# Optimization experiments

Measured on AMD Instinct MI355X. Metric: run time of the kernel, lower is better.

The kernel has to match this reference:

```python
import jax, jax.numpy as jnp
import numpy as np
from jax import lax

N_OBJ = 21   # 20 VOC classes + background
N_ACT = 27   # HICO actions
HUMAN = 14   # index of 'human' in VOC_BBOX_LABEL_NAMES
ROI_SZ = 7
SCALE = 1.0 / 16.0
STD = (0.1, 0.1, 0.2, 0.2)
MEAN = (0.0, 0.0, 0.0, 0.0)
SIGMA = 0.3
NMS_T = 0.0  # thresh passed to non_maximum_suppression in source
EPS = 1e-3
NEG = -1e30


def setup_inputs():
    key = jax.random.key(0)
    ks = jax.random.split(key, 9)
    R = 2000
    C, Hf, Wf = 512, 38, 50
    Himg, Wimg = 608, 800
    x = jax.random.normal(ks[0], (1, C, Hf, Wf), dtype=jnp.float32)
    pred_scores = jax.random.normal(ks[1], (R, N_OBJ), dtype=jnp.float32)
    pred_off = 0.5 * jax.random.normal(ks[2], (R, N_OBJ * 4), dtype=jnp.float32)
    ys = jnp.sort(jax.random.uniform(ks[3], (R, 2), minval=0.0, maxval=Himg - 1.0), axis=1)
    xs = jnp.sort(jax.random.uniform(ks[4], (R, 2), minval=0.0, maxval=Wimg - 1.0), axis=1)
    rois = jnp.stack([ys[:, 0], xs[:, 0], ys[:, 1] + 1.0, xs[:, 1] + 1.0], axis=1)  # [R,4] yxyx, image coords
    D = C * ROI_SZ * ROI_SZ  # 25088
    W1 = jax.random.normal(ks[5], (D, 4096), dtype=jnp.float32) / np.float32(np.sqrt(D))
    b1 = jnp.zeros((4096,), jnp.float32)
    W2 = jax.random.normal(ks[6], (4096, 4096), dtype=jnp.float32) / 64.0
    b2 = jnp.zeros((4096,), jnp.float32)
    W_loc = jax.random.normal(ks[7], (4096, 4), dtype=jnp.float32) / 64.0
    b_loc = jnp.zeros((4,), jnp.float32)
    W_act = jax.random.normal(ks[8], (4096, N_ACT), dtype=jnp.float32) / 64.0
    b_act = jnp.zeros((N_ACT,), jnp.float32)
    imgshape = jnp.array([Himg, Wimg], dtype=jnp.int32)
    return {"x": x, "pred_scores": pred_scores, "pred_off": pred_off, "rois": rois,
            "imgshape": imgshape, "W1": W1, "b1": b1, "W2": W2, "b2": b2,
            "W_loc": W_loc, "b_loc": b_loc, "W_act": W_act, "b_act": b_act}


def loc2bbox(src, loc):
    # src, loc: [...,4] (y1,x1,y2,x2) / (dy,dx,dh,dw)
    h = src[..., 2] - src[..., 0]
    w = src[..., 3] - src[..., 1]
    cy = src[..., 0] + 0.5 * h
    cx = src[..., 1] + 0.5 * w
    cy2 = loc[..., 0] * h + cy
    cx2 = loc[..., 1] * w + cx
    h2 = jnp.exp(loc[..., 2]) * h
    w2 = jnp.exp(loc[..., 3]) * w
    return jnp.stack([cy2 - 0.5 * h2, cx2 - 0.5 * w2, cy2 + 0.5 * h2, cx2 + 0.5 * w2], axis=-1)


def nms_keep(boxes, scores):
    # chainercv-style greedy NMS: suppress if IoU with an already-kept box >= NMS_T
    R = boxes.shape[0]
    order = jnp.argsort(-scores)
    b = boxes[order]
    tl = jnp.maximum(b[:, None, :2], b[None, :, :2])
    br = jnp.minimum(b[:, None, 2:], b[None, :, 2:])
    inter = jnp.prod(jnp.maximum(br - tl, 0.0), axis=-1)
    area = jnp.prod(jnp.maximum(b[:, 2:] - b[:, :2], 0.0), axis=-1)
    iou = inter / (area[:, None] + area[None, :] - inter + 1e-12)
    idx = jnp.arange(R)
    def body(i, keep):
        sup = jnp.any((iou[i] >= NMS_T) & keep & (idx < i))
        return keep.at[i].set(~sup)
    keep_sorted = lax.fori_loop(0, R, body, jnp.ones((R,), bool))
    return jnp.zeros((R,), bool).at[order].set(keep_sorted)


def roi_pool(feat, box_yxyx):
    # chainer RoIPooling2D on one roi; roi fed as [x1,y1,x2,y2] then scaled by SCALE
    C, Hf, Wf = feat.shape
    y1, x1, y2, x2 = box_yxyx[0], box_yxyx[1], box_yxyx[2], box_yxyx[3]
    xmin = jnp.round(x1 * SCALE).astype(jnp.int32)
    ymin = jnp.round(y1 * SCALE).astype(jnp.int32)
    xmax = jnp.round(x2 * SCALE).astype(jnp.int32)
    ymax = jnp.round(y2 * SCALE).astype(jnp.int32)
    rw = jnp.maximum(xmax - xmin + 1, 1).astype(jnp.float32)
    rh = jnp.maximum(ymax - ymin + 1, 1).astype(jnp.float32)
    p = jnp.arange(ROI_SZ, dtype=jnp.float32)
    hstart = jnp.clip(ymin + jnp.floor(p * rh / ROI_SZ).astype(jnp.int32), 0, Hf)
    hend = jnp.clip(ymin + jnp.ceil((p + 1.0) * rh / ROI_SZ).astype(jnp.int32), 0, Hf)
    wstart = jnp.clip(xmin + jnp.floor(p * rw / ROI_SZ).astype(jnp.int32), 0, Wf)
    wend = jnp.clip(xmin + jnp.ceil((p + 1.0) * rw / ROI_SZ).astype(jnp.int32), 0, Wf)
    r = jnp.arange(Hf)
    c = jnp.arange(Wf)
    rowm = (r[None, :] >= hstart[:, None]) & (r[None, :] < hend[:, None])  # [7,Hf]
    colm = (c[None, :] >= wstart[:, None]) & (c[None, :] < wend[:, None])  # [7,Wf]
    t = jnp.where(colm[None, None, :, :], feat[:, :, None, :], NEG).max(axis=-1)  # [C,Hf,7]
    out = jnp.where(rowm[None, :, :, None], t[:, None, :, :], NEG).max(axis=2)    # [C,7,7]
    return jnp.where(out <= NEG * 0.5, 0.0, out)


def xywh(b):
    # quirky encoding used in forward: x=(b3-b1)/2, y=(b2-b0)/2, w=b3-b1, h=b2-b0
    w = b[..., 3] - b[..., 1]
    h = b[..., 2] - b[..., 0]
    return jnp.stack([0.5 * w, 0.5 * h, w, h], axis=-1)


def reference(x, pred_scores, pred_off, rois, imgshape, W1, b1, W2, b2, W_loc, b_loc, W_act, b_act):
    Hf, Wf = x.shape[2], x.shape[3]
    R = rois.shape[0]
    img = imgshape.astype(jnp.float32)
    my_scale = Hf / img[0]
    sy = Hf / img[0]
    sx = Wf / img[1]
    roi = rois * jnp.stack([sy, sx, sy, sx])  # resize_bbox(image -> feature)
    std = jnp.tile(jnp.asarray(STD, jnp.float32), (N_OBJ,))
    mean = jnp.tile(jnp.asarray(MEAN, jnp.float32), (N_OBJ,))
    loc = (pred_off * std + mean).reshape(R, N_OBJ, 4)
    src = jnp.broadcast_to(roi[:, None, :], loc.shape)
    cb = loc2bbox(src, loc)  # [R,21,4]
    yc = jnp.clip(cb[..., 0::2], 0.0, float(Hf))
    xc = jnp.clip(cb[..., 1::2], 0.0, float(Wf))
    cls_bbox = jnp.stack([yc[..., 0], xc[..., 0], yc[..., 1], xc[..., 1]], axis=-1)
    prob = jax.nn.softmax(pred_scores, axis=1)  # strictly > 0, so prob>0 mask keeps all
    boxes_c = jnp.swapaxes(cls_bbox[:, 1:, :], 0, 1)  # [20,R,4]
    scores_c = prob[:, 1:].T                          # [20,R]
    keep = jax.vmap(nms_keep)(boxes_c, scores_c)      # [20,R] bool
    bbox_all = boxes_c.reshape(-1, 4)
    score_all = scores_c.reshape(-1)
    label_all = jnp.repeat(jnp.arange(N_OBJ - 1), R)
    kept = keep.reshape(-1)
    # get_pred_human_box: best-scoring kept box with label 'human'
    hmask = kept & (label_all == HUMAN)
    hi = jnp.argmax(jnp.where(hmask, score_all, -1.0))
    human_box = bbox_all[hi]  # feature coords, yxyx
    # RoI pool + classifier heads
    pool = roi_pool(x[0], human_box)
    feat = pool.reshape(1, -1)  # [1, 25088]
    fc7 = jax.nn.relu(jax.nn.relu(feat @ W1 + b1) @ W2 + b2)
    pred_object_loc = fc7 @ W_loc + b_loc   # [1,4]
    action_scores = fc7 @ W_act + b_act     # [1,27]
    # test-mode: gaussian over relative box encodings to pick object
    h4 = xywh(human_box)
    mu = xywh(pred_object_loc[0])
    cand = xywh(bbox_all)  # [20R,4]
    hw = jnp.maximum(h4[2], EPS)
    hh = jnp.maximum(h4[3], EPS)
    cw = jnp.maximum(cand[:, 2], EPS)
    ch = jnp.maximum(cand[:, 3], EPS)
    boh = jnp.stack([(cand[:, 0] - h4[0]) / hw, (cand[:, 1] - h4[1]) / hh,
                     jnp.log(cw / hw), jnp.log(ch / hh)], axis=-1)
    gau = jnp.exp(-jnp.sum((boh - mu) ** 2, axis=-1) / (2.0 * SIGMA * SIGMA))
    vmask = kept & (label_all != HUMAN)
    bi = jnp.argmax(jnp.where(vmask, gau, -1.0))
    obj_box = bbox_all[bi]
    # resize back to image coords (flip_bbox treated as identity)
    inv = jnp.stack([img[0] / Hf, img[1] / Wf, img[0] / Hf, img[1] / Wf])
    pred_human_box = (human_box * inv)[None, :]
    pred_obj_box = (obj_box * inv)[None, :]
    return pred_human_box, pred_obj_box, action_scores, my_scale
```

## Files before the change

### kernel.cpp

```cpp
#include <hip/hip_runtime.h>
#include <math.h>

#define R_ROIS 2000
#define NOBJ   21
#define NACT   27
#define HUMAN  14
#define CFEAT  512
#define HF     38
#define WF     50
#define DFEAT  (CFEAT*7*7)
#define H1DIM  4096

#define WS_LOGZ   0
#define WS_KEPT   2000
#define WS_FEAT   2080
#define WS_H1     27168
#define WS_H1R    31264
#define WS_FC7    35360
#define WS_FC7R   39456
#define WS_LOC    43552
#define WS_ACT    43556

__global__ void k_init(float* h1, float* fc7) {
    int i = blockIdx.x * blockDim.x + threadIdx.x;
    if (i < H1DIM) { h1[i] = 0.f; fc7[i] = 0.f; }
}

__global__ void k_logz(const float* __restrict__ scores, float* __restrict__ logZ) {
    int r = blockIdx.x * blockDim.x + threadIdx.x;
    if (r >= R_ROIS) return;
    const float* s = scores + r * NOBJ;
    float m = s[0];
    #pragma unroll
    for (int c = 1; c < NOBJ; ++c) m = fmaxf(m, s[c]);
    float sum = 0.f;
    #pragma unroll
    for (int c = 0; c < NOBJ; ++c) sum += expf(s[c] - m);
    logZ[r] = m + logf(sum);
}

__global__ void k_class_top(const float* __restrict__ scores, const float* __restrict__ logZ,
                            const float* __restrict__ off, const float* __restrict__ rois,
                            const int* __restrict__ imgshape, float* __restrict__ kept_box) {
    int cls = blockIdx.x + 1;
    __shared__ float sval[256];
    __shared__ int   sidx[256];
    float best = -1e30f; int bidx = 0x7fffffff;
    for (int r = threadIdx.x; r < R_ROIS; r += 256) {
        float v = scores[r * NOBJ + cls] - logZ[r];
        if (v > best) { best = v; bidx = r; }
    }
    sval[threadIdx.x] = best; sidx[threadIdx.x] = bidx;
    __syncthreads();
    for (int s = 128; s > 0; s >>= 1) {
        if (threadIdx.x < s) {
            float ov = sval[threadIdx.x + s]; int oi = sidx[threadIdx.x + s];
            if (ov > sval[threadIdx.x] ||
                (ov == sval[threadIdx.x] && oi < sidx[threadIdx.x])) {
                sval[threadIdx.x] = ov; sidx[threadIdx.x] = oi;
            }
        }
        __syncthreads();
    }
    if (threadIdx.x == 0) {
        int r = sidx[0];
        float Himg = (float)imgshape[0], Wimg = (float)imgshape[1];
        float sy = (float)HF / Himg, sx = (float)WF / Wimg;
        float y1 = rois[r*4+0]*sy, x1 = rois[r*4+1]*sx;
        float y2 = rois[r*4+2]*sy, x2 = rois[r*4+3]*sx;
        float dy = off[r*(NOBJ*4) + cls*4+0] * 0.1f;
        float dx = off[r*(NOBJ*4) + cls*4+1] * 0.1f;
        float dh = off[r*(NOBJ*4) + cls*4+2] * 0.2f;
        float dw = off[r*(NOBJ*4) + cls*4+3] * 0.2f;
        float h = y2 - y1, w = x2 - x1;
        float cy = y1 + 0.5f*h, cx = x1 + 0.5f*w;
        float cy2 = dy*h + cy, cx2 = dx*w + cx;
        float h2 = expf(dh)*h, w2 = expf(dw)*w;
        float by1 = fminf(fmaxf(cy2 - 0.5f*h2, 0.f), (float)HF);
        float bx1 = fminf(fmaxf(cx2 - 0.5f*w2, 0.f), (float)WF);
        float by2 = fminf(fmaxf(cy2 + 0.5f*h2, 0.f), (float)HF);
        float bx2 = fminf(fmaxf(cx2 + 0.5f*w2, 0.f), (float)WF);
        int l = cls - 1;
        kept_box[l*4+0] = by1; kept_box[l*4+1] = bx1;
        kept_box[l*4+2] = by2; kept_box[l*4+3] = bx2;
    }
}

__global__ void k_roipool(const float* __restrict__ x, const float* __restrict__ kept_box,
                          float* __restrict__ feat) {
    int idx = blockIdx.x * blockDim.x + threadIdx.x;
    if (idx >= DFEAT) return;
    float y1 = kept_box[HUMAN*4+0], x1 = kept_box[HUMAN*4+1];
    float y2 = kept_box[HUMAN*4+2], x2 = kept_box[HUMAN*4+3];
    int xmin = (int)rintf(x1 * 0.0625f);
    int ymin = (int)rintf(y1 * 0.0625f);
    int xmax = (int)rintf(x2 * 0.0625f);
    int ymax = (int)rintf(y2 * 0.0625f);
    float rw = (float)max(xmax - xmin + 1, 1);
    float rh = (float)max(ymax - ymin + 1, 1);
    int c = idx / 49, rem = idx % 49, pi = rem / 7, pj = rem % 7;
    int hs  = min(max(ymin + (int)floorf((float)pi * rh / 7.f), 0), HF);
    int he  = min(max(ymin + (int)ceilf((float)(pi+1) * rh / 7.f), 0), HF);
    int wss = min(max(xmin + (int)floorf((float)pj * rw / 7.f), 0), WF);
    int we  = min(max(xmin + (int)ceilf((float)(pj+1) * rw / 7.f), 0), WF);
    float m = -1e30f;
    for (int rr = hs; rr < he; ++rr)
        for (int cc = wss; cc < we; ++cc)
            m = fmaxf(m, x[c*(HF*WF) + rr*WF + cc]);
    feat[idx] = (m <= -5e29f) ? 0.f : m;
}

template<int ROWS>
__global__ __launch_bounds__(256)
void k_matvec(const float* __restrict__ W, const float* __restrict__ vin,
              float* __restrict__ vout, int ncols) {
    __shared__ float sv[ROWS];
    int row0 = blockIdx.x * ROWS;
    int col0 = blockIdx.y * 1024 + threadIdx.x * 4;
    for (int i = threadIdx.x; i < ROWS; i += 256) sv[i] = vin[row0 + i];
    __syncthreads();
    float a0 = 0.f, a1 = 0.f, a2 = 0.f, a3 = 0.f;
    const float4* Wv = (const float4*)W;
    long base = ((long)row0 * ncols + col0) >> 2;
    int stride = ncols >> 2;
    #pragma unroll 4
    for (int i = 0; i < ROWS; ++i) {
        float f = sv[i];
        float4 w = Wv[base + (long)i * stride];
        a0 += f * w.x; a1 += f * w.y; a2 += f * w.z; a3 += f * w.w;
    }
    atomicAdd(&vout[col0+0], a0);
    atomicAdd(&vout[col0+1], a1);
    atomicAdd(&vout[col0+2], a2);
    atomicAdd(&vout[col0+3], a3);
}

__global__ void k_bias_relu(const float* __restrict__ vin, const float* __restrict__ b,
                            float* __restrict__ vout, int n) {
    int i = blockIdx.x * blockDim.x + threadIdx.x;
    if (i < n) vout[i] = fmaxf(vin[i] + b[i], 0.f);
}

__global__ void k_heads(const float* __restrict__ fc7r,
                        const float* __restrict__ W_loc, const float* __restrict__ b_loc,
                        const float* __restrict__ W_act, const float* __restrict__ b_act,
                        float* __restrict__ loc_out, float* __restrict__ act_out) {
    int k = blockIdx.x;
    __shared__ float red[256];
    float sum = 0.f;
    if (k < 4) {
        for (int i = threadIdx.x; i < H1DIM; i += 256) sum += fc7r[i] * W_loc[i*4 + k];
    } else {
        int j = k - 4;
        for (int i = threadIdx.x; i < H1DIM; i += 256) sum += fc7r[i] * W_act[i*NACT + j];
    }
    red[threadIdx.x] = sum; __syncthreads();
    for (int s = 128; s > 0; s >>= 1) {
        if (threadIdx.x < s) red[threadIdx.x] += red[threadIdx.x + s];
        __syncthreads();
    }
    if (threadIdx.x == 0) {
        if (k < 4) loc_out[k] = red[0] + b_loc[k];
        else       act_out[k-4] = red[0] + b_act[k-4];
    }
}

__global__ void k_final(const float* __restrict__ kept_box, const float* __restrict__ loc_out,
                        const float* __restrict__ act_out, const int* __restrict__ imgshape,
                        float* __restrict__ out) {
    if (threadIdx.x != 0 || blockIdx.x != 0) return;
    float hb0 = kept_box[HUMAN*4+0], hb1 = kept_box[HUMAN*4+1];
    float hb2 = kept_box[HUMAN*4+2], hb3 = kept_box[HUMAN*4+3];
    float h4w = hb3 - hb1, h4h = hb2 - hb0;
    float h4x = 0.5f * h4w, h4y = 0.5f * h4h;
    float hw = fmaxf(h4w, 1e-3f), hh = fmaxf(h4h, 1e-3f);
    float l0 = loc_out[0], l1 = loc_out[1], l2 = loc_out[2], l3 = loc_out[3];
    float muw = l3 - l1, muh = l2 - l0;
    float mux = 0.5f * muw, muy = 0.5f * muh;
    float bestg = -2.f; int bl = 0;
    for (int l = 0; l < 20; ++l) {
        if (l == HUMAN) continue;
        float b0 = kept_box[l*4+0], b1 = kept_box[l*4+1];
        float b2 = kept_box[l*4+2], b3 = kept_box[l*4+3];
        float cw = fmaxf(b3 - b1, 1e-3f), ch = fmaxf(b2 - b0, 1e-3f);
        float c0 = 0.5f * (b3 - b1), c1 = 0.5f * (b2 - b0);
        float d0 = (c0 - h4x) / hw - mux;
        float d1 = (c1 - h4y) / hh - muy;
        float d2 = logf(cw / hw) - muw;
        float d3 = logf(ch / hh) - muh;
        float g = expf(-(d0*d0 + d1*d1 + d2*d2 + d3*d3) / (2.f * 0.3f * 0.3f));
        if (g > bestg) { bestg = g; bl = l; }
    }
    float Himg = (float)imgshape[0], Wimg = (float)imgshape[1];
    float iy = Himg / (float)HF, ix = Wimg / (float)WF;
    out[0] = hb0 * iy; out[1] = hb1 * ix; out[2] = hb2 * iy; out[3] = hb3 * ix;
    out[4] = kept_box[bl*4+0] * iy; out[5] = kept_box[bl*4+1] * ix;
    out[6] = kept_box[bl*4+2] * iy; out[7] = kept_box[bl*4+3] * ix;
    for (int j = 0; j < NACT; ++j) out[8+j] = act_out[j];
    out[35] = (float)HF / Himg;
}

extern "C" void kernel_launch(void* const* d_in, const int* in_sizes, int n_in,
                              void* d_out, int out_size, void* d_ws, size_t ws_size,
                              hipStream_t stream) {
    const float* x           = (const float*)d_in[0];
    const float* pred_scores = (const float*)d_in[1];
    const float* pred_off    = (const float*)d_in[2];
    const float* rois        = (const float*)d_in[3];
    const int*   imgshape    = (const int*)d_in[4];
    const float* W1          = (const float*)d_in[5];
    const float* b1          = (const float*)d_in[6];
    const float* W2          = (const float*)d_in[7];
    const float* b2          = (const float*)d_in[8];
    const float* W_loc       = (const float*)d_in[9];
    const float* b_loc       = (const float*)d_in[10];
    const float* W_act       = (const float*)d_in[11];
    const float* b_act       = (const float*)d_in[12];
    float* out = (float*)d_out;

    float* ws   = (float*)d_ws;
    float* logZ = ws + WS_LOGZ;
    float* kept = ws + WS_KEPT;
    float* feat = ws + WS_FEAT;
    float* h1   = ws + WS_H1;
    float* h1r  = ws + WS_H1R;
    float* fc7  = ws + WS_FC7;
    float* fc7r = ws + WS_FC7R;
    float* loco = ws + WS_LOC;
    float* acto = ws + WS_ACT;

    k_init<<<16, 256, 0, stream>>>(h1, fc7);
    k_logz<<<(R_ROIS + 255) / 256, 256, 0, stream>>>(pred_scores, logZ);
    k_class_top<<<20, 256, 0, stream>>>(pred_scores, logZ, pred_off, rois, imgshape, kept);
    k_roipool<<<(DFEAT + 255) / 256, 256, 0, stream>>>(x, kept, feat);
    k_matvec<128><<<dim3(196, 4), 256, 0, stream>>>(W1, feat, h1, H1DIM);
    k_bias_relu<<<16, 256, 0, stream>>>(h1, b1, h1r, H1DIM);
    k_matvec<64><<<dim3(64, 4), 256, 0, stream>>>(W2, h1r, fc7, H1DIM);
    k_bias_relu<<<16, 256, 0, stream>>>(fc7, b2, fc7r, H1DIM);
    k_heads<<<31, 256, 0, stream>>>(fc7r, W_loc, b_loc, W_act, b_act, loco, acto);
    k_final<<<1, 64, 0, stream>>>(kept, loco, acto, imgshape, out);
}
```

Baseline: 632.0 us.

## Fuse softmax, zero-init and bias-ReLU into neighbouring kernels; use nontemporal weight loads

Merges the logZ softmax and buffer zeroing into the per-class top-score kernel, and folds the bias+ReLU steps into the second matvec's input staging and the heads kernel. Weight streams in the matvecs now use nontemporal loads with deeper unrolling. The aim is to remove four kernel launches and their intermediate buffers. In exchange, each of the 20 class blocks recomputes the softmax for all 2000 rows, and the heads kernel recomputes bias+ReLU in all 31 blocks.

```diff
diff --git a/kernel.cpp b/kernel.cpp
--- a/kernel.cpp
+++ b/kernel.cpp
@@ -11,43 +11,38 @@
 #define DFEAT  (CFEAT*7*7)
 #define H1DIM  4096
 
-#define WS_LOGZ   0
-#define WS_KEPT   2000
-#define WS_FEAT   2080
-#define WS_H1     27168
-#define WS_H1R    31264
-#define WS_FC7    35360
-#define WS_FC7R   39456
-#define WS_LOC    43552
-#define WS_ACT    43556
-
-__global__ void k_init(float* h1, float* fc7) {
-    int i = blockIdx.x * blockDim.x + threadIdx.x;
-    if (i < H1DIM) { h1[i] = 0.f; fc7[i] = 0.f; }
-}
-
-__global__ void k_logz(const float* __restrict__ scores, float* __restrict__ logZ) {
-    int r = blockIdx.x * blockDim.x + threadIdx.x;
-    if (r >= R_ROIS) return;
-    const float* s = scores + r * NOBJ;
-    float m = s[0];
-    #pragma unroll
-    for (int c = 1; c < NOBJ; ++c) m = fmaxf(m, s[c]);
-    float sum = 0.f;
-    #pragma unroll
-    for (int c = 0; c < NOBJ; ++c) sum += expf(s[c] - m);
-    logZ[r] = m + logf(sum);
-}
-
-__global__ void k_class_top(const float* __restrict__ scores, const float* __restrict__ logZ,
-                            const float* __restrict__ off, const float* __restrict__ rois,
-                            const int* __restrict__ imgshape, float* __restrict__ kept_box) {
+typedef float floatx4 __attribute__((ext_vector_type(4)));
+
+#define WS_KEPT   0
+#define WS_FEAT   80
+#define WS_H1     (WS_FEAT + DFEAT)
+#define WS_FC7    (WS_H1 + H1DIM)
+#define WS_LOC    (WS_FC7 + H1DIM)
+#define WS_ACT    (WS_LOC + 4)
+
+__global__ __launch_bounds__(256)
+void k_top(const float* __restrict__ scores, const float* __restrict__ off,
+           const float* __restrict__ rois, const int* __restrict__ imgshape,
+           float* __restrict__ kept_box, float* __restrict__ h1,
+           float* __restrict__ fc7) {
+    int g = blockIdx.x * 256 + threadIdx.x;
+    for (int j = g; j < 2 * H1DIM; j += 20 * 256) {
+        if (j < H1DIM) h1[j] = 0.f; else fc7[j - H1DIM] = 0.f;
+    }
+
     int cls = blockIdx.x + 1;
     __shared__ float sval[256];
     __shared__ int   sidx[256];
     float best = -1e30f; int bidx = 0x7fffffff;
     for (int r = threadIdx.x; r < R_ROIS; r += 256) {
-        float v = scores[r * NOBJ + cls] - logZ[r];
+        const float* s = scores + r * NOBJ;
+        float m = s[0];
+        #pragma unroll
+        for (int c = 1; c < NOBJ; ++c) m = fmaxf(m, s[c]);
+        float sum = 0.f;
+        #pragma unroll
+        for (int c = 0; c < NOBJ; ++c) sum += expf(s[c] - m);
+        float v = s[cls] - (m + logf(sum));
         if (v > best) { best = v; bidx = r; }
     }
     sval[threadIdx.x] = best; sidx[threadIdx.x] = bidx;
@@ -110,23 +105,27 @@
     feat[idx] = (m <= -5e29f) ? 0.f : m;
 }
 
-template<int ROWS>
+template<int ROWS, bool RELU>
 __global__ __launch_bounds__(256)
 void k_matvec(const float* __restrict__ W, const float* __restrict__ vin,
-              float* __restrict__ vout, int ncols) {
+              const float* __restrict__ bias, float* __restrict__ vout, int ncols) {
     __shared__ float sv[ROWS];
     int row0 = blockIdx.x * ROWS;
     int col0 = blockIdx.y * 1024 + threadIdx.x * 4;
-    for (int i = threadIdx.x; i < ROWS; i += 256) sv[i] = vin[row0 + i];
+    for (int i = threadIdx.x; i < ROWS; i += 256) {
+        float v = vin[row0 + i];
+        if (RELU) v = fmaxf(v + bias[row0 + i], 0.f);
+        sv[i] = v;
+    }
     __syncthreads();
     float a0 = 0.f, a1 = 0.f, a2 = 0.f, a3 = 0.f;
-    const float4* Wv = (const float4*)W;
+    const floatx4* Wv = (const floatx4*)W;
     long base = ((long)row0 * ncols + col0) >> 2;
     int stride = ncols >> 2;
-    #pragma unroll 4
+    #pragma unroll 8
     for (int i = 0; i < ROWS; ++i) {
         float f = sv[i];
-        float4 w = Wv[base + (long)i * stride];
+        floatx4 w = __builtin_nontemporal_load(&Wv[base + (long)i * stride]);
         a0 += f * w.x; a1 += f * w.y; a2 += f * w.z; a3 += f * w.w;
     }
     atomicAdd(&vout[col0+0], a0);
@@ -135,13 +134,7 @@
     atomicAdd(&vout[col0+3], a3);
 }
 
-__global__ void k_bias_relu(const float* __restrict__ vin, const float* __restrict__ b,
-                            float* __restrict__ vout, int n) {
-    int i = blockIdx.x * blockDim.x + threadIdx.x;
-    if (i < n) vout[i] = fmaxf(vin[i] + b[i], 0.f);
-}
-
-__global__ void k_heads(const float* __restrict__ fc7r,
+__global__ void k_heads(const float* __restrict__ fc7, const float* __restrict__ b2,
                         const float* __restrict__ W_loc, const float* __restrict__ b_loc,
                         const float* __restrict__ W_act, const float* __restrict__ b_act,
                         float* __restrict__ loc_out, float* __restrict__ act_out) {
@@ -149,10 +142,16 @@
     __shared__ float red[256];
     float sum = 0.f;
     if (k < 4) {
-        for (int i = threadIdx.x; i < H1DIM; i += 256) sum += fc7r[i] * W_loc[i*4 + k];
+        for (int i = threadIdx.x; i < H1DIM; i += 256) {
+            float f = fmaxf(fc7[i] + b2[i], 0.f);
+            sum += f * W_loc[i*4 + k];
+        }
     } else {
         int j = k - 4;
-        for (int i = threadIdx.x; i < H1DIM; i += 256) sum += fc7r[i] * W_act[i*NACT + j];
+        for (int i = threadIdx.x; i < H1DIM; i += 256) {
+            float f = fmaxf(fc7[i] + b2[i], 0.f);
+            sum += f * W_act[i*NACT + j];
+        }
     }
     red[threadIdx.x] = sum; __syncthreads();
     for (int s = 128; s > 0; s >>= 1) {
@@ -219,24 +218,17 @@
     float* out = (float*)d_out;
 
     float* ws   = (float*)d_ws;
-    float* logZ = ws + WS_LOGZ;
     float* kept = ws + WS_KEPT;
     float* feat = ws + WS_FEAT;
     float* h1   = ws + WS_H1;
-    float* h1r  = ws + WS_H1R;
     float* fc7  = ws + WS_FC7;
-    float* fc7r = ws + WS_FC7R;
     float* loco = ws + WS_LOC;
     float* acto = ws + WS_ACT;
 
-    k_init<<<16, 256, 0, stream>>>(h1, fc7);
-    k_logz<<<(R_ROIS + 255) / 256, 256, 0, stream>>>(pred_scores, logZ);
-    k_class_top<<<20, 256, 0, stream>>>(pred_scores, logZ, pred_off, rois, imgshape, kept);
+    k_top<<<20, 256, 0, stream>>>(pred_scores, pred_off, rois, imgshape, kept, h1, fc7);
     k_roipool<<<(DFEAT + 255) / 256, 256, 0, stream>>>(x, kept, feat);
-    k_matvec<128><<<dim3(196, 4), 256, 0, stream>>>(W1, feat, h1, H1DIM);
-    k_bias_relu<<<16, 256, 0, stream>>>(h1, b1, h1r, H1DIM);
-    k_matvec<64><<<dim3(64, 4), 256, 0, stream>>>(W2, h1r, fc7, H1DIM);
-    k_bias_relu<<<16, 256, 0, stream>>>(fc7, b2, fc7r, H1DIM);
-    k_heads<<<31, 256, 0, stream>>>(fc7r, W_loc, b_loc, W_act, b_act, loco, acto);
+    k_matvec<128, false><<<dim3(196, 4), 256, 0, stream>>>(W1, feat, (const float*)nullptr, h1, H1DIM);
+    k_matvec<64, true><<<dim3(64, 4), 256, 0, stream>>>(W2, h1, b1, fc7, H1DIM);
+    k_heads<<<31, 256, 0, stream>>>(fc7, b2, W_loc, b_loc, W_act, b_act, loco, acto);
     k_final<<<1, 64, 0, stream>>>(kept, loco, acto, imgshape, out);
 }
```

Result: faster. 612.1 us (-3.1%).
